# Performance work log

Measured on AMD Instinct MI355X. Metric: run time of the kernel, lower is better.

Reference implementation:

```python
import jax, jax.numpy as jnp
import numpy as np

N = 10000      # nodes (attention_adj_matrix_shape = (N, N))
E = 320000     # edges, avg degree 32
D_IN = 256     # input feature dim
D_H = 256      # hidden_units = [256]
ALPHA = 0.2    # leaky_relu slope for attention activation


def setup_inputs() -> dict:
    key = jax.random.key(0)
    k_x, k_src, k_dst, k_w1, k_b1, k_wa, k_ba = jax.random.split(key, 7)
    node_features = jax.random.normal(k_x, (N, D_IN), dtype=jnp.float32)
    # edges sorted by source column (tf.math.segment_sum requires sorted segment ids)
    src = jnp.sort(jax.random.randint(k_src, (E,), 0, N))
    dst = jax.random.randint(k_dst, (E,), 0, N)
    edges = jnp.stack([src, dst], axis=1).astype(jnp.int64)
    # hidden_layer: single Dense(256) (linear, keras Dense default activation=None)
    W1 = jax.random.normal(k_w1, (D_IN, D_H), dtype=jnp.float32) / np.sqrt(D_IN)
    b1 = jnp.zeros((D_H,), dtype=jnp.float32)
    # attention_layer: Dense(1) then activation
    Wa = jax.random.normal(k_wa, (2 * D_H, 1), dtype=jnp.float32) / np.sqrt(2 * D_H)
    ba = jnp.zeros((1,), dtype=jnp.float32)
    return {"node_features": node_features, "edges": edges,
            "W1": W1, "b1": b1, "Wa": Wa, "ba": ba}


def reference(node_features, edges, W1, b1, Wa, ba):
    n = node_features.shape[0]
    # hidden projection
    feats = node_features @ W1 + b1                       # [N, D_H]
    src, dst = edges[:, 0], edges[:, 1]
    # pairwise gather + concat: [E, 2*D_H]
    pair = jnp.concatenate([feats[src], feats[dst]], axis=1)
    scores = jax.nn.leaky_relu((pair @ Wa + ba)[:, 0], ALPHA)  # [E]
    # segment softmax over source node (matches exp / segment_sum / gather)
    ex = jnp.exp(scores)
    denom = jax.ops.segment_sum(ex, src, num_segments=n)       # [N]
    alpha = ex / denom[src]                                     # [E]
    # dense scatter of attention weights (scatter_nd sums duplicates)
    A = jnp.zeros((n, n), dtype=feats.dtype).at[src, dst].add(alpha)
    # add_self_features=False -> plain aggregate
    return A @ feats                                            # [N, D_H]
```

## Files before the change

### kernel.cpp

```cpp
#include <hip/hip_runtime.h>
#include <hip/hip_bf16.h>

#define N_NODES 10000
#define E_EDGES 320000
#define D 256
#define LRELU_ALPHA 0.2f


using short8  = __attribute__((ext_vector_type(8))) short;
using floatx4 = __attribute__((ext_vector_type(4))) float;
using bf16 = __hip_bfloat16;

__device__ __forceinline__ float bu2f(unsigned short u) {
    return __uint_as_float((unsigned)u << 16);
}
__device__ __forceinline__ unsigned short f2bu(float f) {
    union { bf16 b; unsigned short u; } cv;
    cv.b = __float2bfloat16(f);
    return cv.u;
}

__global__ __launch_bounds__(256) void wprep(const float* __restrict__ W1,
                                             bf16* __restrict__ W1f) {
    const int id = blockIdx.x * 256 + threadIdx.x;
    const int j = id & 7, l = (id >> 3) & 63, t = (id >> 9) & 15, s = id >> 13;
    const int k = s * 32 + (l >> 4) * 8 + j;
    const int n = t * 16 + (l & 15);
    W1f[id] = __float2bfloat16(W1[k * D + n]);
}

__global__ __launch_bounds__(256) void gemm_mfma(const float* __restrict__ X,
                                                 const bf16* __restrict__ W1f,
                                                 const float* __restrict__ b1,
                                                 const float* __restrict__ Wa,
                                                 bf16* __restrict__ featsb,
                                                 float* __restrict__ a_src,
                                                 float* __restrict__ a_dst) {
    const int w = threadIdx.x >> 6, l = threadIdx.x & 63;
    const int quad = l >> 4, lan = l & 15;
    const int row0 = blockIdx.x * 16;

    floatx4 acc[4] = {{0.f, 0.f, 0.f, 0.f}, {0.f, 0.f, 0.f, 0.f},
                      {0.f, 0.f, 0.f, 0.f}, {0.f, 0.f, 0.f, 0.f}};

    const float4* Ax = (const float4*)(X + (size_t)(row0 + lan) * D);
    const short8* B8 = (const short8*)W1f;

    #pragma unroll
    for (int s = 0; s < 8; ++s) {
        const float4 u = Ax[s * 8 + quad * 2];
        const float4 v = Ax[s * 8 + quad * 2 + 1];
        short8 af;
        af[0] = (short)f2bu(u.x); af[1] = (short)f2bu(u.y);
        af[2] = (short)f2bu(u.z); af[3] = (short)f2bu(u.w);
        af[4] = (short)f2bu(v.x); af[5] = (short)f2bu(v.y);
        af[6] = (short)f2bu(v.z); af[7] = (short)f2bu(v.w);
        #pragma unroll
        for (int t = 0; t < 4; ++t) {
            const short8 bf = B8[(s * 16 + (4 * w + t)) * 64 + l];
            acc[t] = __builtin_amdgcn_mfma_f32_16x16x32_bf16(af, bf, acc[t], 0, 0, 0);
        }
    }

    float p1[4] = {0.f, 0.f, 0.f, 0.f}, p2[4] = {0.f, 0.f, 0.f, 0.f};
    #pragma unroll
    for (int t = 0; t < 4; ++t) {
        const int n = (4 * w + t) * 16 + lan;
        const float bias = b1[n], wa1 = Wa[n], wa2 = Wa[D + n];
        #pragma unroll
        for (int r = 0; r < 4; ++r) {
            const float v = acc[t][r] + bias;
            featsb[(size_t)(row0 + quad * 4 + r) * D + n] = __float2bfloat16(v);
            p1[r] += v * wa1;
            p2[r] += v * wa2;
        }
    }

    __shared__ float red1[4][16], red2[4][16];
    #pragma unroll
    for (int r = 0; r < 4; ++r) {
        #pragma unroll
        for (int off = 1; off < 16; off <<= 1) {
            p1[r] += __shfl_xor(p1[r], off);
            p2[r] += __shfl_xor(p2[r], off);
        }
        if (lan == 0) { red1[w][quad * 4 + r] = p1[r]; red2[w][quad * 4 + r] = p2[r]; }
    }
    __syncthreads();
    if (threadIdx.x < 16) {
        const int m = threadIdx.x;
        a_src[row0 + m] = red1[0][m] + red1[1][m] + red1[2][m] + red1[3][m];
        a_dst[row0 + m] = red2[0][m] + red2[1][m] + red2[2][m] + red2[3][m];
    }
}

__global__ __launch_bounds__(256) void prep(const int* __restrict__ raw,
                                            const float* __restrict__ a_src,
                                            const float* __restrict__ a_dst,
                                            const float* __restrict__ ba,
                                            int2* __restrict__ edata,
                                            int* __restrict__ row_start) {
    bool is64 = true;
    #pragma unroll
    for (int t = 0; t < 16; ++t)
        if (raw[2 * t + 1] != 0) is64 = false;

    int e = blockIdx.x * 256 + threadIdx.x;
    if (e >= E_EDGES) return;
    int s, d, sprev;
    if (is64) { s = raw[4 * e]; d = raw[4 * e + 2]; sprev = e ? raw[4 * e - 4] : -1; }
    else      { s = raw[2 * e]; d = raw[2 * e + 1]; sprev = e ? raw[2 * e - 2] : -1; }

    float sc = a_src[s] + a_dst[d] + ba[0];
    sc = (sc > 0.f) ? sc : LRELU_ALPHA * sc;
    edata[e] = make_int2(d << 9, __float_as_int(expf(sc)));

    for (int r = sprev + 1; r <= s; ++r) row_start[r] = e;
    if (e == E_EDGES - 1)
        for (int r = s + 1; r <= N_NODES; ++r) row_start[r] = E_EDGES;
}

__global__ __launch_bounds__(256) void aggregate(const int2* __restrict__ edata,
                                                 const int* __restrict__ row_start,
                                                 const unsigned short* __restrict__ featsb,
                                                 float* __restrict__ out) {
    __shared__ int2 els[4][64];
    const int wv = threadIdx.x >> 6, l = threadIdx.x & 63;
    const int i = blockIdx.x * 4 + wv;
    const int rs = row_start[i], re = row_start[i + 1];
    const char* Fb = (const char*)featsb;

    float4 acc = {0.f, 0.f, 0.f, 0.f};
    float dsum = 0.f;

    for (int e = rs; e < re; e += 64) {
        const int cnt = min(64, re - e);
        if (l < cnt) els[wv][l] = edata[e + l];
        __builtin_amdgcn_wave_barrier();

        int j = 0;
        for (; j + 8 <= cnt; j += 8) {
            #pragma unroll
            for (int u = 0; u < 8; ++u) {
                const int2 ed = els[wv][j + u];
                const ushort4 f = *(const ushort4*)(Fb + (size_t)(unsigned)ed.x + l * 8);
                const float x = __int_as_float(ed.y);
                acc.x += x * bu2f(f.x); acc.y += x * bu2f(f.y);
                acc.z += x * bu2f(f.z); acc.w += x * bu2f(f.w);
                dsum += x;
            }
        }
        for (; j < cnt; ++j) {
            const int2 ed = els[wv][j];
            const ushort4 f = *(const ushort4*)(Fb + (size_t)(unsigned)ed.x + l * 8);
            const float x = __int_as_float(ed.y);
            acc.x += x * bu2f(f.x); acc.y += x * bu2f(f.y);
            acc.z += x * bu2f(f.z); acc.w += x * bu2f(f.w);
            dsum += x;
        }
        __builtin_amdgcn_wave_barrier();
    }

    const float inv = (re > rs) ? 1.f / dsum : 0.f;
    float4 o;
    o.x = acc.x * inv; o.y = acc.y * inv; o.z = acc.z * inv; o.w = acc.w * inv;
    ((float4*)out)[(size_t)i * 64 + l] = o;
}

extern "C" void kernel_launch(void* const* d_in, const int* in_sizes, int n_in,
                              void* d_out, int out_size, void* d_ws, size_t ws_size,
                              hipStream_t stream) {
    const float* X     = (const float*)d_in[0];
    const int*   edges = (const int*)d_in[1];
    const float* W1    = (const float*)d_in[2];
    const float* b1    = (const float*)d_in[3];
    const float* Wa    = (const float*)d_in[4];
    const float* ba    = (const float*)d_in[5];
    float* out = (float*)d_out;

    bf16* featsb = (bf16*)d_ws;
    bf16* W1f    = featsb + (size_t)N_NODES * D;
    float* a_src = (float*)(W1f + 65536);
    float* a_dst = a_src + N_NODES;
    int2*  edata = (int2*)(a_dst + N_NODES);
    int*   row_start = (int*)(edata + E_EDGES);

    wprep<<<65536 / 256, 256, 0, stream>>>(W1, W1f);
    gemm_mfma<<<N_NODES / 16, 256, 0, stream>>>(X, W1f, b1, Wa, featsb, a_src, a_dst);
    prep<<<(E_EDGES + 255) / 256, 256, 0, stream>>>(edges, a_src, a_dst, ba, edata, row_start);
    aggregate<<<N_NODES / 4, 256, 0, stream>>>(edata, row_start,
                                               (const unsigned short*)featsb, out);
}
```

Baseline: 103.3 us.

## Fuse weight prep with CSR build and compute edge scores inside aggregate

```diff
diff --git a/kernel.cpp b/kernel.cpp
--- a/kernel.cpp
+++ b/kernel.cpp
@@ -8,6 +8,7 @@
 
 
 using short8  = __attribute__((ext_vector_type(8))) short;
+using ushort8 = __attribute__((ext_vector_type(8))) unsigned short;
 using floatx4 = __attribute__((ext_vector_type(4))) float;
 using bf16 = __hip_bfloat16;
 
@@ -20,13 +21,33 @@
     return cv.u;
 }
 
-__global__ __launch_bounds__(256) void wprep(const float* __restrict__ W1,
-                                             bf16* __restrict__ W1f) {
-    const int id = blockIdx.x * 256 + threadIdx.x;
-    const int j = id & 7, l = (id >> 3) & 63, t = (id >> 9) & 15, s = id >> 13;
-    const int k = s * 32 + (l >> 4) * 8 + j;
-    const int n = t * 16 + (l & 15);
-    W1f[id] = __float2bfloat16(W1[k * D + n]);
+__global__ __launch_bounds__(256) void prep_fused(const float* __restrict__ W1,
+                                                  bf16* __restrict__ W1f,
+                                                  const int* __restrict__ raw,
+                                                  int* __restrict__ row_start,
+                                                  int* __restrict__ flag) {
+    const int b = blockIdx.x;
+    if (b < 256) {
+        const int id = b * 256 + threadIdx.x;
+        const int j = id & 7, l = (id >> 3) & 63, t = (id >> 9) & 15, s = id >> 13;
+        const int k = s * 32 + (l >> 4) * 8 + j;
+        const int n = t * 16 + (l & 15);
+        W1f[id] = __float2bfloat16(W1[k * D + n]);
+        return;
+    }
+    bool is64 = true;
+    #pragma unroll
+    for (int t = 0; t < 16; ++t)
+        if (raw[2 * t + 1] != 0) is64 = false;
+    const int e = (b - 256) * 256 + threadIdx.x;
+    if (e >= E_EDGES) return;
+    if (e == 0) *flag = is64 ? 1 : 0;
+    int s, sprev;
+    if (is64) { s = raw[4 * e]; sprev = e ? raw[4 * e - 4] : -1; }
+    else      { s = raw[2 * e]; sprev = e ? raw[2 * e - 2] : -1; }
+    for (int r = sprev + 1; r <= s; ++r) row_start[r] = e;
+    if (e == E_EDGES - 1)
+        for (int r = s + 1; r <= N_NODES; ++r) row_start[r] = E_EDGES;
 }
 
 __global__ __launch_bounds__(256) void gemm_mfma(const float* __restrict__ X,
@@ -94,77 +115,73 @@
     }
 }
 
-__global__ __launch_bounds__(256) void prep(const int* __restrict__ raw,
-                                            const float* __restrict__ a_src,
-                                            const float* __restrict__ a_dst,
-                                            const float* __restrict__ ba,
-                                            int2* __restrict__ edata,
-                                            int* __restrict__ row_start) {
-    bool is64 = true;
-    #pragma unroll
-    for (int t = 0; t < 16; ++t)
-        if (raw[2 * t + 1] != 0) is64 = false;
-
-    int e = blockIdx.x * 256 + threadIdx.x;
-    if (e >= E_EDGES) return;
-    int s, d, sprev;
-    if (is64) { s = raw[4 * e]; d = raw[4 * e + 2]; sprev = e ? raw[4 * e - 4] : -1; }
-    else      { s = raw[2 * e]; d = raw[2 * e + 1]; sprev = e ? raw[2 * e - 2] : -1; }
-
-    float sc = a_src[s] + a_dst[d] + ba[0];
-    sc = (sc > 0.f) ? sc : LRELU_ALPHA * sc;
-    edata[e] = make_int2(d << 9, __float_as_int(expf(sc)));
-
-    for (int r = sprev + 1; r <= s; ++r) row_start[r] = e;
-    if (e == E_EDGES - 1)
-        for (int r = s + 1; r <= N_NODES; ++r) row_start[r] = E_EDGES;
-}
-
-__global__ __launch_bounds__(256) void aggregate(const int2* __restrict__ edata,
+__global__ __launch_bounds__(256) void aggregate(const int* __restrict__ raw,
                                                  const int* __restrict__ row_start,
+                                                 const int* __restrict__ flag,
+                                                 const float* __restrict__ a_src,
+                                                 const float* __restrict__ a_dst,
+                                                 const float* __restrict__ ba,
                                                  const unsigned short* __restrict__ featsb,
                                                  float* __restrict__ out) {
     __shared__ int2 els[4][64];
     const int wv = threadIdx.x >> 6, l = threadIdx.x & 63;
+    const int half = l >> 5, lh = l & 31;
     const int i = blockIdx.x * 4 + wv;
     const int rs = row_start[i], re = row_start[i + 1];
-    const char* Fb = (const char*)featsb;
-
-    float4 acc = {0.f, 0.f, 0.f, 0.f};
+    const bool is64 = (*flag) != 0;
+    const float base = a_src[i] + ba[0];
+    const char* Fbl = (const char*)featsb + lh * 16;
+
+    float acc[8] = {0.f, 0.f, 0.f, 0.f, 0.f, 0.f, 0.f, 0.f};
     float dsum = 0.f;
 
-    for (int e = rs; e < re; e += 64) {
-        const int cnt = min(64, re - e);
-        if (l < cnt) els[wv][l] = edata[e + l];
+    for (int e0 = rs; e0 < re; e0 += 64) {
+        const int cnt = min(64, re - e0);
+        if (l < cnt) {
+            const int ee = e0 + l;
+            const int d = is64 ? raw[4 * ee + 2] : raw[2 * ee + 1];
+            float sc = base + a_dst[d];
+            sc = (sc > 0.f) ? sc : LRELU_ALPHA * sc;
+            els[wv][l] = make_int2(d << 9, __float_as_int(expf(sc)));
+        } else if (l < ((cnt + 1) & ~1)) {
+            els[wv][l] = make_int2(0, 0);
+        }
         __builtin_amdgcn_wave_barrier();
 
+        const int pairs = (cnt + 1) >> 1;
         int j = 0;
-        for (; j + 8 <= cnt; j += 8) {
-            #pragma unroll
-            for (int u = 0; u < 8; ++u) {
-                const int2 ed = els[wv][j + u];
-                const ushort4 f = *(const ushort4*)(Fb + (size_t)(unsigned)ed.x + l * 8);
-                const float x = __int_as_float(ed.y);
-                acc.x += x * bu2f(f.x); acc.y += x * bu2f(f.y);
-                acc.z += x * bu2f(f.z); acc.w += x * bu2f(f.w);
-                dsum += x;
-            }
-        }
-        for (; j < cnt; ++j) {
-            const int2 ed = els[wv][j];
-            const ushort4 f = *(const ushort4*)(Fb + (size_t)(unsigned)ed.x + l * 8);
-            const float x = __int_as_float(ed.y);
-            acc.x += x * bu2f(f.x); acc.y += x * bu2f(f.y);
-            acc.z += x * bu2f(f.z); acc.w += x * bu2f(f.w);
-            dsum += x;
-        }
+        #define PAIR(idx) do {                                                \
+            const int2 ed = els[wv][2 * (idx) + half];                        \
+            const ushort8 f = *(const ushort8*)(Fbl + (size_t)(unsigned)ed.x);\
+            const float x = __int_as_float(ed.y);                             \
+            acc[0] += x * bu2f(f[0]); acc[1] += x * bu2f(f[1]);               \
+            acc[2] += x * bu2f(f[2]); acc[3] += x * bu2f(f[3]);               \
+            acc[4] += x * bu2f(f[4]); acc[5] += x * bu2f(f[5]);               \
+            acc[6] += x * bu2f(f[6]); acc[7] += x * bu2f(f[7]);               \
+            dsum += x;                                                        \
+        } while (0)
+        for (; j + 4 <= pairs; j += 4) {
+            PAIR(j); PAIR(j + 1); PAIR(j + 2); PAIR(j + 3);
+        }
+        for (; j < pairs; ++j) PAIR(j);
+        #undef PAIR
         __builtin_amdgcn_wave_barrier();
     }
 
+    #pragma unroll
+    for (int r = 0; r < 8; ++r) acc[r] += __shfl_xor(acc[r], 32);
+    dsum += __shfl_xor(dsum, 32);
+
     const float inv = (re > rs) ? 1.f / dsum : 0.f;
-    float4 o;
-    o.x = acc.x * inv; o.y = acc.y * inv; o.z = acc.z * inv; o.w = acc.w * inv;
-    ((float4*)out)[(size_t)i * 64 + l] = o;
+    if (l < 32) {
+        float4 o0, o1;
+        o0.x = acc[0] * inv; o0.y = acc[1] * inv;
+        o0.z = acc[2] * inv; o0.w = acc[3] * inv;
+        o1.x = acc[4] * inv; o1.y = acc[5] * inv;
+        o1.z = acc[6] * inv; o1.w = acc[7] * inv;
+        float4* op = (float4*)(out + (size_t)i * D + lh * 8);
+        op[0] = o0; op[1] = o1;
+    }
 }
 
 extern "C" void kernel_launch(void* const* d_in, const int* in_sizes, int n_in,
@@ -182,12 +199,13 @@
     bf16* W1f    = featsb + (size_t)N_NODES * D;
     float* a_src = (float*)(W1f + 65536);
     float* a_dst = a_src + N_NODES;
-    int2*  edata = (int2*)(a_dst + N_NODES);
-    int*   row_start = (int*)(edata + E_EDGES);
-
-    wprep<<<65536 / 256, 256, 0, stream>>>(W1, W1f);
+    int*   row_start = (int*)(a_dst + N_NODES);
+    int*   flag  = row_start + N_NODES + 1;
+
+    prep_fused<<<256 + (E_EDGES + 255) / 256, 256, 0, stream>>>(W1, W1f, edges,
+                                                               row_start, flag);
     gemm_mfma<<<N_NODES / 16, 256, 0, stream>>>(X, W1f, b1, Wa, featsb, a_src, a_dst);
-    prep<<<(E_EDGES + 255) / 256, 256, 0, stream>>>(edges, a_src, a_dst, ba, edata, row_start);
-    aggregate<<<N_NODES / 4, 256, 0, stream>>>(edata, row_start,
+    aggregate<<<N_NODES / 4, 256, 0, stream>>>(edges, row_start, flag,
+                                               a_src, a_dst, ba,
                                                (const unsigned short*)featsb, out);
 }
```

Measured after the change: 100.5 us, median of 2. -2.8%, faster.
